# Kernel tuning notes

Hardware: AMD Instinct MI355X
Metric: run time of the kernel (lower is better)

## Reference

```python
import jax, jax.numpy as jnp
import numpy as np

B = 2048      # env batch (graphs)
A = 8         # agents per graph (fully connected)
N = B * A     # total nodes
DIN = 192     # raw obs dim
HD = 256      # h_dim (base MLP)
MD = 256      # mem_dim (GRU)
GD = 128      # gnn_dim (per-head GATv2 out, concat=False -> head mean)
H = 4         # GAT heads
NA = 20       # n_actions
ED = 3        # edge_dim


def setup_inputs() -> dict:
    key = jax.random.key(0)
    ks = jax.random.split(key, 16)
    # fully-connected directed graph per group of A agents, no self loops
    s, d = np.meshgrid(np.arange(A), np.arange(A), indexing='ij')
    mask = s != d
    s = s[mask]; d = d[mask]                     # [A*(A-1)]
    off = (np.arange(B) * A)[:, None]
    src = (off + s[None, :]).reshape(-1)
    dst = (off + d[None, :]).reshape(-1)
    edge_index = jnp.asarray(np.stack([src, dst]), dtype=jnp.int32)  # [2, E]
    E = src.shape[0]
    p = lambda k, sh: jax.random.normal(ks[k], sh, jnp.float32) * 0.02
    return {
        'inputs': jax.random.normal(ks[0], (N, DIN), jnp.float32),
        'hidden_states': jax.random.normal(ks[1], (N, MD), jnp.float32) * 0.1,
        'edge_index': edge_index,
        'edge_attr': jax.random.uniform(ks[2], (E, ED), jnp.float32),
        # base MLP (2 layers: Linear+ReLU+LayerNorm)
        'W1': p(3, (DIN, HD)), 'b1': jnp.zeros(HD), 'g1': jnp.ones(HD), 'be1': jnp.zeros(HD),
        'W2': p(4, (HD, HD)),  'b2': jnp.zeros(HD), 'g2': jnp.ones(HD), 'be2': jnp.zeros(HD),
        # GRUCell
        'Wih': p(5, (3 * MD, HD)), 'Whh': p(6, (3 * MD, MD)),
        'bih': jnp.zeros(3 * MD), 'bhh': jnp.zeros(3 * MD),
        # GATv2Conv (edge_dim=3, heads=4, concat=False, residual)
        'Wl': p(7, (MD, H * GD)), 'bl': jnp.zeros(H * GD),
        'Wr': p(8, (MD, H * GD)), 'br': jnp.zeros(H * GD),
        'att': p(9, (H, GD)),
        'We': p(10, (ED, H * GD)),
        'Wres': p(11, (MD, GD)),
        'bg': jnp.zeros(GD),
        # head: LayerNorm + Linear
        'lng': jnp.ones(GD), 'lnb': jnp.zeros(GD),
        'Wout': p(12, (GD, NA)), 'bout': jnp.zeros(NA),
    }


def _ln(x, g, b):
    mu = jnp.mean(x, -1, keepdims=True)
    xc = x - mu
    v = jnp.mean(xc * xc, -1, keepdims=True)
    return xc * jax.lax.rsqrt(v + 1e-5) * g + b


def _fwd(inputs, hidden_states, edge_attr, edge_index,
         W1, b1, g1, be1, W2, b2, g2, be2,
         Wih, Whh, bih, bhh,
         Wl, bl, Wr, br, att, We, Wres, bg,
         lng, lnb, Wout, bout):
    src, dst = edge_index[0], edge_index[1]
    # ---- base MLP encode ----
    x = _ln(jax.nn.relu(inputs @ W1 + b1), g1, be1)
    x = _ln(jax.nn.relu(x @ W2 + b2), g2, be2)          # [N, HD]
    # ---- SimpleConv(aggr='mean', combine_root='self_loop') ----
    s = jax.ops.segment_sum(x[src], dst, num_segments=N) + x
    deg = jax.ops.segment_sum(jnp.ones(src.shape[0], x.dtype), dst, num_segments=N) + 1.0
    x = s / deg[:, None]                                 # [N, HD]
    # ---- GRUCell ----
    gi = x @ Wih.T + bih
    gh = hidden_states @ Whh.T + bhh
    ir, iz, inn = jnp.split(gi, 3, -1)
    hr, hz, hn = jnp.split(gh, 3, -1)
    r = jax.nn.sigmoid(ir + hr)
    z = jax.nn.sigmoid(iz + hz)
    n = jnp.tanh(inn + r * hn)
    h = (1.0 - z) * n + z * hidden_states                # [N, MD]
    # ---- GATv2Conv (add self loops, edge_attr fill='mean') ----
    loop = jnp.arange(N, dtype=src.dtype)
    sf = jnp.concatenate([src, loop])
    df = jnp.concatenate([dst, loop])
    ea = jnp.concatenate([edge_attr, jnp.broadcast_to(edge_attr.mean(0), (N, ED))], 0)
    xl = (h @ Wl + bl).reshape(N, H, GD)
    xr = (h @ Wr + br).reshape(N, H, GD)
    m = xl[sf] + xr[df] + (ea @ We).reshape(-1, H, GD)   # [Ef, H, GD]
    m = jnp.where(m > 0, m, 0.2 * m)                     # leaky_relu(0.2)
    logits = jnp.einsum('ehc,hc->eh', m, att)            # [Ef, H]
    mx = jax.ops.segment_max(logits, df, num_segments=N)
    ex = jnp.exp(logits - mx[df])
    den = jax.ops.segment_sum(ex, df, num_segments=N)
    alpha = ex / (den[df] + 1e-16)                       # segment softmax
    out = jax.ops.segment_sum(xl[sf] * alpha[..., None], df, num_segments=N)
    out = out.mean(1) + h @ Wres + bg                    # head mean + residual + bias
    zg = jax.nn.relu(out)                                # [N, GD]
    # ---- action head ----
    q = _ln(zg, lng, lnb) @ Wout + bout                  # [N, NA]
    return q, h


def reference(inputs, hidden_states, edge_index, edge_attr,
              W1, b1, g1, be1, W2, b2, g2, be2,
              Wih, Whh, bih, bhh,
              Wl, bl, Wr, br, att, We, Wres, bg,
              lng, lnb, Wout, bout):
    return _fwd(inputs, hidden_states, edge_attr, edge_index,
                W1, b1, g1, be1, W2, b2, g2, be2,
                Wih, Whh, bih, bhh,
                Wl, bl, Wr, br, att, We, Wres, bg,
                lng, lnb, Wout, bout)
```

## Files before the change

### kernel.cpp

```cpp
#include <hip/hip_runtime.h>
#include <hip/hip_bf16.h>

constexpr int NB  = 2048;
constexpr int AG  = 8;
constexpr int NN  = NB * AG;
constexpr int DIN = 192;
constexpr int HD  = 256;
constexpr int MD  = 256;
constexpr int GD  = 128;
constexpr int NA  = 20;
constexpr int NE  = NB * AG * (AG - 1);

typedef __attribute__((ext_vector_type(8))) short bfrag8;
typedef __attribute__((ext_vector_type(4))) short sfrag4;
typedef __attribute__((ext_vector_type(4))) float f32x4;

#define MFMA16(a, b, c) __builtin_amdgcn_mfma_f32_16x16x32_bf16((a), (b), (c), 0, 0, 0)

__device__ __forceinline__ float bf2f(__hip_bfloat16 x) { return __bfloat162float(x); }
__device__ __forceinline__ __hip_bfloat16 f2bf(float x) { return __float2bfloat16(x); }
__device__ __forceinline__ short f2bs(float x) {
    __hip_bfloat16 b = __float2bfloat16(x);
    return *reinterpret_cast<short*>(&b);
}
__device__ __forceinline__ bfrag8 ldf(const __hip_bfloat16* p) { return *(const bfrag8*)p; }
__device__ __forceinline__ bfrag8 ldf32(const float* p) {
    const f32x4 a = *(const f32x4*)p;
    const f32x4 b = *(const f32x4*)(p + 4);
    bfrag8 r;
    r[0] = f2bs(a[0]); r[1] = f2bs(a[1]); r[2] = f2bs(a[2]); r[3] = f2bs(a[3]);
    r[4] = f2bs(b[0]); r[5] = f2bs(b[1]); r[6] = f2bs(b[2]); r[7] = f2bs(b[3]);
    return r;
}
__device__ __forceinline__ float sigmf(float x) { return 1.f / (1.f + __expf(-x)); }
__device__ __forceinline__ float blo(unsigned u) { return __uint_as_float(u << 16); }
__device__ __forceinline__ float bhi(unsigned u) { return __uint_as_float(u & 0xffff0000u); }

__global__ __launch_bounds__(256) void k_prep(
    const float* __restrict__ W1, const float* __restrict__ W2,
    const float* __restrict__ Wih, const float* __restrict__ Whh,
    const float* __restrict__ Wl, const float* __restrict__ bl,
    const float* __restrict__ Wr, const float* __restrict__ br,
    const float* __restrict__ Wres, const float* __restrict__ Wout,
    const float* __restrict__ ea,
    __hip_bfloat16* __restrict__ W1T, __hip_bfloat16* __restrict__ W2T,
    __hip_bfloat16* __restrict__ WihB, __hip_bfloat16* __restrict__ WhhB,
    __hip_bfloat16* __restrict__ WcatT, float* __restrict__ WoutTf,
    float* __restrict__ bcat, float* __restrict__ ea_partials)
{
    __shared__ float sw[4][3];
    const int tid = threadIdx.x;
    if (blockIdx.x >= 3151) {
        const int b = blockIdx.x - 3151;
        float a0 = 0.f, a1 = 0.f, a2 = 0.f;
#pragma unroll
        for (int k = 0; k < 7; k++) {
            int e = b * 1792 + k * 256 + tid;
            a0 += ea[e * 3 + 0];
            a1 += ea[e * 3 + 1];
            a2 += ea[e * 3 + 2];
        }
#pragma unroll
        for (int off = 1; off < 64; off <<= 1) {
            a0 += __shfl_xor(a0, off); a1 += __shfl_xor(a1, off); a2 += __shfl_xor(a2, off);
        }
        if ((tid & 63) == 0) { sw[tid >> 6][0] = a0; sw[tid >> 6][1] = a1; sw[tid >> 6][2] = a2; }
        __syncthreads();
        if (tid == 0) {
            ea_partials[b * 3 + 0] = sw[0][0] + sw[1][0] + sw[2][0] + sw[3][0];
            ea_partials[b * 3 + 1] = sw[0][1] + sw[1][1] + sw[2][1] + sw[3][1];
            ea_partials[b * 3 + 2] = sw[0][2] + sw[1][2] + sw[2][2] + sw[3][2];
        }
        return;
    }
    int i = blockIdx.x * 256 + tid;
    if (i < 49152) { int o = i / 192, c = i % 192; W1T[i] = f2bf(W1[c * 256 + o]); return; }
    i -= 49152;
    if (i < 65536) { int o = i >> 8, c = i & 255; W2T[i] = f2bf(W2[c * 256 + o]); return; }
    i -= 65536;
    if (i < 196608) { WihB[i] = f2bf(Wih[i]); return; }
    i -= 196608;
    if (i < 196608) { WhhB[i] = f2bf(Whh[i]); return; }
    i -= 196608;
    if (i < 294912) {
        int o = i >> 8, c = i & 255;
        float v;
        if (o < 512)       v = Wl[c * 512 + o];
        else if (o < 1024) v = Wr[c * 512 + (o - 512)];
        else               v = Wres[c * 128 + (o - 1024)];
        WcatT[i] = f2bf(v); return;
    }
    i -= 294912;
    if (i < 2560) { int o = i >> 7, c = i & 127; WoutTf[i] = Wout[c * 20 + o]; return; }
    i -= 2560;
    if (i < 1152) {
        float v = 0.f;
        if (i < 512) v = bl[i]; else if (i < 1024) v = br[i - 512];
        bcat[i] = v;
    }
}

__global__ __launch_bounds__(256) void k_encode(
    const float* __restrict__ in,
    const __hip_bfloat16* __restrict__ W1T,
    const float* __restrict__ b1, const float* __restrict__ g1, const float* __restrict__ be1,
    const __hip_bfloat16* __restrict__ W2T,
    const float* __restrict__ b2, const float* __restrict__ g2, const float* __restrict__ be2,
    __hip_bfloat16* __restrict__ xm)
{
    __shared__ float sf[16][257];
    __shared__ alignas(16) __hip_bfloat16 sb[16][264];
    const int tid = threadIdx.x;
    const int lane = tid & 63, w = tid >> 6;
    const int r = lane & 15, q = lane >> 4;
    const int m0 = blockIdx.x * 16;

    {
        bfrag8 af[6];
        const float* ap = in + (size_t)(m0 + r) * DIN + q * 8;
#pragma unroll
        for (int kb = 0; kb < 6; kb++) af[kb] = ldf32(ap + kb * 32);
#pragma unroll
        for (int i = 0; i < 4; i++) {
            int t = w * 4 + i;
            const __hip_bfloat16* wp = W1T + (size_t)(t * 16 + r) * DIN + q * 8;
            bfrag8 bf[6];
#pragma unroll
            for (int kb = 0; kb < 6; kb++) bf[kb] = ldf(wp + kb * 32);
            f32x4 acc = (f32x4){0.f, 0.f, 0.f, 0.f};
#pragma unroll
            for (int kb = 0; kb < 6; kb++) acc = MFMA16(af[kb], bf[kb], acc);
            int col = t * 16 + r;
            float bias = b1[col];
#pragma unroll
            for (int reg = 0; reg < 4; reg++)
                sf[q * 4 + reg][col] = fmaxf(acc[reg] + bias, 0.f);
        }
    }
    __syncthreads();
    {
        int rowi = tid >> 4, c16 = tid & 15;
        float vals[16]; float s = 0.f, s2 = 0.f;
#pragma unroll
        for (int j = 0; j < 16; j++) { float v = sf[rowi][c16 + 16 * j]; vals[j] = v; s += v; s2 += v * v; }
#pragma unroll
        for (int off = 1; off < 16; off <<= 1) { s += __shfl_xor(s, off); s2 += __shfl_xor(s2, off); }
        float mean = s * (1.f / HD);
        float var = fmaxf(s2 * (1.f / HD) - mean * mean, 0.f);
        float rs = rsqrtf(var + 1e-5f);
#pragma unroll
        for (int j = 0; j < 16; j++) {
            int col = c16 + 16 * j;
            sb[rowi][col] = f2bf((vals[j] - mean) * rs * g1[col] + be1[col]);
        }
    }
    __syncthreads();

    {
        bfrag8 af[8];
        const __hip_bfloat16* ap = &sb[r][0];
#pragma unroll
        for (int kb = 0; kb < 8; kb++) af[kb] = ldf(ap + kb * 32 + q * 8);
        float outv[4][4];
#pragma unroll
        for (int i = 0; i < 4; i++) {
            int t = w * 4 + i;
            const __hip_bfloat16* wp = W2T + (size_t)(t * 16 + r) * HD + q * 8;
            bfrag8 bf[8];
#pragma unroll
            for (int kb = 0; kb < 8; kb++) bf[kb] = ldf(wp + kb * 32);
            f32x4 acc = (f32x4){0.f, 0.f, 0.f, 0.f};
#pragma unroll
            for (int kb = 0; kb < 8; kb++) acc = MFMA16(af[kb], bf[kb], acc);
#pragma unroll
            for (int reg = 0; reg < 4; reg++) outv[i][reg] = acc[reg];
        }
        __syncthreads();
#pragma unroll
        for (int i = 0; i < 4; i++) {
            int col = (w * 4 + i) * 16 + r;
            float bias = b2[col];
#pragma unroll
            for (int reg = 0; reg < 4; reg++)
                sf[q * 4 + reg][col] = fmaxf(outv[i][reg] + bias, 0.f);
        }
    }
    __syncthreads();
    {
        int rowi = tid >> 4, c16 = tid & 15;
        float vals[16]; float s = 0.f, s2 = 0.f;
#pragma unroll
        for (int j = 0; j < 16; j++) { float v = sf[rowi][c16 + 16 * j]; vals[j] = v; s += v; s2 += v * v; }
#pragma unroll
        for (int off = 1; off < 16; off <<= 1) { s += __shfl_xor(s, off); s2 += __shfl_xor(s2, off); }
        float mean = s * (1.f / HD);
        float var = fmaxf(s2 * (1.f / HD) - mean * mean, 0.f);
        float rs = rsqrtf(var + 1e-5f);
#pragma unroll
        for (int j = 0; j < 16; j++) {
            int col = c16 + 16 * j;
            sb[rowi][col] = f2bf((vals[j] - mean) * rs * g2[col] + be2[col]);
        }
    }
    __syncthreads();
    {
        int col = tid;
        float a0 = 0.f, a1 = 0.f;
#pragma unroll
        for (int i = 0; i < 8; i++) { a0 += bf2f(sb[i][col]); a1 += bf2f(sb[8 + i][col]); }
        xm[(size_t)(2 * blockIdx.x) * HD + col] = f2bf(a0 * 0.125f);
        xm[(size_t)(2 * blockIdx.x + 1) * HD + col] = f2bf(a1 * 0.125f);
    }
}

__global__ __launch_bounds__(256) void k_gi(
    const __hip_bfloat16* __restrict__ xm,
    const __hip_bfloat16* __restrict__ WihB,
    const float* __restrict__ bih,
    float* __restrict__ gi)
{
    const int tid = threadIdx.x;
    const int lane = tid & 63, w = tid >> 6;
    const int r = lane & 15, q = lane >> 4;
    const int m0 = (blockIdx.x >> 1) * 16;
    const int t0 = (blockIdx.x & 1) * 24;

    bfrag8 af[8];
    const __hip_bfloat16* ap = xm + (size_t)(m0 + r) * MD + q * 8;
#pragma unroll
    for (int kb = 0; kb < 8; kb++) af[kb] = ldf(ap + kb * 32);
#pragma unroll
    for (int i = 0; i < 6; i++) {
        int t = t0 + w * 6 + i;
        const __hip_bfloat16* wp = WihB + (size_t)(t * 16 + r) * MD + q * 8;
        bfrag8 bf[8];
#pragma unroll
        for (int kb = 0; kb < 8; kb++) bf[kb] = ldf(wp + kb * 32);
        f32x4 acc = (f32x4){0.f, 0.f, 0.f, 0.f};
#pragma unroll
        for (int kb = 0; kb < 8; kb++) acc = MFMA16(af[kb], bf[kb], acc);
        int col = t * 16 + r;
        float bias = bih[col];
#pragma unroll
        for (int reg = 0; reg < 4; reg++) {
            int R = m0 + q * 4 + reg;
            gi[(size_t)R * 768 + col] = acc[reg] + bias;
        }
    }
}

__global__ __launch_bounds__(256, 3) void k_gatgru(
    const float* __restrict__ hprev,
    const __hip_bfloat16* __restrict__ WhhB,
    const float* __restrict__ bhh,
    const float* __restrict__ gi,
    const __hip_bfloat16* __restrict__ WcatT,
    const float* __restrict__ bcat,
    const float* __restrict__ ea,
    const float* __restrict__ ea_partials,
    const float* __restrict__ att,
    const float* __restrict__ We,
    const float* __restrict__ bg,
    const float* __restrict__ lng, const float* __restrict__ lnb,
    const float* __restrict__ WoutTf,
    const float* __restrict__ bout,
    float* __restrict__ hout,
    float* __restrict__ qout)
{
    __shared__ alignas(16) __hip_bfloat16 sx[16][1160];
    __shared__ alignas(16) unsigned char u_shszg[16 * 272 * 2];
    __shared__ float slog[2][4][8][8];
    __shared__ float smean[4];
    auto sh  = (__hip_bfloat16(*)[272])u_shszg;
    auto szg = (float(*)[136])u_shszg;
    const int tid = threadIdx.x;
    const int lane = tid & 63, w = tid >> 6;
    const int r = lane & 15, q = lane >> 4;
    const int m0 = blockIdx.x * 16;

    if (tid < 3) {
        float s = 0.f;
        for (int i = 0; i < 64; i++) s += ea_partials[i * 3 + tid];
        smean[tid] = s * (1.f / NE);
    }

    float vea[2][3];
    {
        int l = (lane < 56) ? lane : 0;
#pragma unroll
        for (int g = 0; g < 2; g++) {
            const float* ep = ea + (size_t)((blockIdx.x * 2 + g) * 56 + l) * 3;
            vea[g][0] = ep[0]; vea[g][1] = ep[1]; vea[g][2] = ep[2];
        }
    }

    {
        f32x4 aR[4], aZ[4], aN[4];
#pragma unroll
        for (int i = 0; i < 4; i++) {
            aR[i] = (f32x4){0.f, 0.f, 0.f, 0.f};
            aZ[i] = (f32x4){0.f, 0.f, 0.f, 0.f};
            aN[i] = (f32x4){0.f, 0.f, 0.f, 0.f};
        }
        const float* ap = hprev + (size_t)(m0 + r) * MD + q * 8;
#pragma unroll
        for (int kb = 0; kb < 8; kb++) {
            bfrag8 af = ldf32(ap + kb * 32);
#pragma unroll
            for (int i = 0; i < 4; i++) {
                int ct = w * 4 + i;
                bfrag8 bR = ldf(WhhB + (size_t)(ct * 16 + r) * MD + kb * 32 + q * 8);
                bfrag8 bZ = ldf(WhhB + (size_t)(256 + ct * 16 + r) * MD + kb * 32 + q * 8);
                bfrag8 bN = ldf(WhhB + (size_t)(512 + ct * 16 + r) * MD + kb * 32 + q * 8);
                aR[i] = MFMA16(af, bR, aR[i]);
                aZ[i] = MFMA16(af, bZ, aZ[i]);
                aN[i] = MFMA16(af, bN, aN[i]);
            }
        }
#pragma unroll
        for (int i = 0; i < 4; i++) {
            int c = (w * 4 + i) * 16 + r;
            float bhr = bhh[c], bhz = bhh[256 + c], bhn = bhh[512 + c];
#pragma unroll
            for (int reg = 0; reg < 4; reg++) {
                int R = m0 + q * 4 + reg;
                const float* gir = gi + (size_t)(R >> 3) * 768;
                float rr = sigmf(gir[c] + aR[i][reg] + bhr);
                float zz = sigmf(gir[256 + c] + aZ[i][reg] + bhz);
                float nn = tanhf(gir[512 + c] + rr * (aN[i][reg] + bhn));
                float hp = hprev[(size_t)R * MD + c];
                float hv = (1.f - zz) * nn + zz * hp;
                hout[(size_t)R * MD + c] = hv;
                sh[q * 4 + reg][c] = f2bf(hv);
            }
        }
    }
    __syncthreads();

    {
        bfrag8 afr[8];
#pragma unroll
        for (int kb = 0; kb < 8; kb++) afr[kb] = ldf(&sh[r][kb * 32 + q * 8]);
#pragma unroll
        for (int pass = 0; pass < 2; pass++) {
            f32x4 acc[9];
#pragma unroll
            for (int i = 0; i < 9; i++) acc[i] = (f32x4){0.f, 0.f, 0.f, 0.f};
#pragma unroll
            for (int kb = 0; kb < 8; kb++) {
#pragma unroll
                for (int i = 0; i < 9; i++) {
                    int t = pass * 36 + w * 9 + i;
                    bfrag8 bfv = ldf(WcatT + (size_t)(t * 16 + r) * MD + kb * 32 + q * 8);
                    acc[i] = MFMA16(bfv, afr[kb], acc[i]);
                }
            }
#pragma unroll
            for (int i = 0; i < 9; i++) {
                int fbase = (pass * 36 + w * 9 + i) * 16 + q * 4;
                sfrag4 pk;
#pragma unroll
                for (int reg = 0; reg < 4; reg++)
                    pk[reg] = f2bs(acc[i][reg] + bcat[fbase + reg]);
                *(sfrag4*)&sx[r][fbase] = pk;
            }
        }
    }
    __syncthreads();
    const float em0 = smean[0], em1 = smean[1], em2 = smean[2];

    {
        const int li = lane & 31, half = lane >> 5;
#pragma unroll
        for (int t = 0; t < 2; t++) {
            const int combo = w * 2 + t;
            const int gg = combo >> 2, hh = combo & 3;
            const f32x4 va  = *(const f32x4*)&att[hh * 128 + li * 4];
            const f32x4 vw0 = *(const f32x4*)&We[0 * 512 + hh * 128 + li * 4];
            const f32x4 vw1 = *(const f32x4*)&We[1 * 512 + hh * 128 + li * 4];
            const f32x4 vw2 = *(const f32x4*)&We[2 * 512 + hh * 128 + li * 4];
            float at0 = va[0],  at1 = va[1],  at2 = va[2],  at3 = va[3];
            float w00 = vw0[0], w01 = vw0[1], w02 = vw0[2], w03 = vw0[3];
            float w10 = vw1[0], w11 = vw1[1], w12 = vw1[2], w13 = vw1[3];
            float w20 = vw2[0], w21 = vw2[1], w22 = vw2[2], w23 = vw2[3];
            float ve0 = vea[gg][0], ve1 = vea[gg][1], ve2 = vea[gg][2];
            float xv[4][4];
#pragma unroll
            for (int sh2 = 0; sh2 < 4; sh2++) {
                int sL = sh2 * 2 + half;
                uint2 uxl = *(const uint2*)&sx[gg * 8 + sL][hh * 128 + li * 4];
                xv[sh2][0] = blo(uxl.x); xv[sh2][1] = bhi(uxl.x);
                xv[sh2][2] = blo(uxl.y); xv[sh2][3] = bhi(uxl.y);
            }
            float mylog = 0.f;
#pragma unroll
            for (int d = 0; d < 8; d++) {
                uint2 uxr = *(const uint2*)&sx[gg * 8 + d][512 + hh * 128 + li * 4];
                float xr0 = blo(uxr.x), xr1 = bhi(uxr.x), xr2 = blo(uxr.y), xr3 = bhi(uxr.y);
#pragma unroll
                for (int sh2 = 0; sh2 < 4; sh2++) {
                    int sL = sh2 * 2 + half;
                    int el = sL * 7 + d - (d > sL ? 1 : 0);
                    float e0 = __shfl(ve0, el), e1 = __shfl(ve1, el), e2 = __shfl(ve2, el);
                    bool slf = (sL == d);
                    e0 = slf ? em0 : e0; e1 = slf ? em1 : e1; e2 = slf ? em2 : e2;
                    float p, m;
                    m = fmaf(e2, w20, fmaf(e1, w10, fmaf(e0, w00, xv[sh2][0]))) + xr0;
                    m = fmaxf(m, 0.2f * m); p = m * at0;
                    m = fmaf(e2, w21, fmaf(e1, w11, fmaf(e0, w01, xv[sh2][1]))) + xr1;
                    m = fmaxf(m, 0.2f * m); p = fmaf(m, at1, p);
                    m = fmaf(e2, w22, fmaf(e1, w12, fmaf(e0, w02, xv[sh2][2]))) + xr2;
                    m = fmaxf(m, 0.2f * m); p = fmaf(m, at2, p);
                    m = fmaf(e2, w23, fmaf(e1, w13, fmaf(e0, w03, xv[sh2][3]))) + xr3;
                    m = fmaxf(m, 0.2f * m); p = fmaf(m, at3, p);
                    p += __shfl_xor(p, 1);  p += __shfl_xor(p, 2);  p += __shfl_xor(p, 4);
                    p += __shfl_xor(p, 8);  p += __shfl_xor(p, 16);
                    float got = __shfl(p, ((lane & 1) << 5) | li);
                    bool want = ((lane >> 3) == d) && (((lane & 7) >> 1) == sh2);
                    mylog = want ? got : mylog;
                }
            }
            ((float*)&slog[gg][hh][0][0])[lane] = mylog;
        }
    }
    __syncthreads();

    if (tid < 64) {
        int sg = tid >> 5, sh2 = (tid >> 3) & 3, d = tid & 7;
        float* L = &slog[sg][sh2][d][0];
        float mx = L[0];
#pragma unroll
        for (int s = 1; s < 8; s++) mx = fmaxf(mx, L[s]);
        float ex[8]; float den = 0.f;
#pragma unroll
        for (int s = 0; s < 8; s++) { ex[s] = __expf(L[s] - mx); den += ex[s]; }
        float inv = 1.f / (den + 1e-16f);
#pragma unroll
        for (int s = 0; s < 8; s++) L[s] = ex[s] * inv;
    }
    __syncthreads();

    {
        f32x4 acc0 = (f32x4){0.f, 0.f, 0.f, 0.f};
        f32x4 acc1 = (f32x4){0.f, 0.f, 0.f, 0.f};
        const int ggr = r >> 3, dr = r & 7;
#pragma unroll
        for (int ah = 0; ah < 4; ah++) {
            bfrag8 afA;
#pragma unroll
            for (int j = 0; j < 8; j++) {
                int k = q * 8 + j;
                float v = 0.f;
                if (k < 16) {
                    int ggk = k >> 3, s = k & 7;
                    if (ggk == ggr) v = slog[ggk][ah][dr][s];
                }
                afA[j] = f2bs(v);
            }
#pragma unroll
            for (int j2 = 0; j2 < 2; j2++) {
                int chunk = w * 2 + j2;
                bfrag8 bfB;
#pragma unroll
                for (int j = 0; j < 8; j++) {
                    int k = (q * 8 + j) & 15;
                    bfB[j] = *(const short*)&sx[k][ah * 128 + chunk * 16 + r];
                }
                if (j2 == 0) acc0 = MFMA16(afA, bfB, acc0);
                else         acc1 = MFMA16(afA, bfB, acc1);
            }
        }
#pragma unroll
        for (int j2 = 0; j2 < 2; j2++) {
            f32x4 a = j2 ? acc1 : acc0;
            int c = (w * 2 + j2) * 16 + r;
            float bgc = bg[c];
#pragma unroll
            for (int reg = 0; reg < 4; reg++) {
                int row = q * 4 + reg;
                float o = a[reg] * 0.25f + bf2f(sx[row][1024 + c]) + bgc;
                szg[row][c] = fmaxf(o, 0.f);
            }
        }
    }
    __syncthreads();

    {
        int row = tid >> 4, j = tid & 15;
        float v[8]; float s = 0.f, s2 = 0.f;
#pragma unroll
        for (int cj = 0; cj < 8; cj++) { v[cj] = szg[row][j + 16 * cj]; s += v[cj]; s2 += v[cj] * v[cj]; }
#pragma unroll
        for (int off = 1; off < 16; off <<= 1) { s += __shfl_xor(s, off); s2 += __shfl_xor(s2, off); }
        float mean = s * (1.f / GD);
        float var = fmaxf(s2 * (1.f / GD) - mean * mean, 0.f);
        float rs = rsqrtf(var + 1e-5f);
#pragma unroll
        for (int cj = 0; cj < 8; cj++) {
            int c = j + 16 * cj;
            szg[row][c] = (v[cj] - mean) * rs * lng[c] + lnb[c];
        }
    }
    __syncthreads();

    {
        int row = tid >> 4, j = tid & 15;
        for (int jj = j; jj < NA; jj += 16) {
            float a = bout[jj];
            const float* wo = WoutTf + jj * 128;
#pragma unroll
            for (int c4 = 0; c4 < 32; c4++) {
                f32x4 z = *(const f32x4*)&szg[row][c4 * 4];
                const f32x4 wv = *(const f32x4*)&wo[c4 * 4];
                a = fmaf(z[0], wv[0], a); a = fmaf(z[1], wv[1], a);
                a = fmaf(z[2], wv[2], a); a = fmaf(z[3], wv[3], a);
            }
            qout[(size_t)(m0 + row) * NA + jj] = a;
        }
    }
}

extern "C" void kernel_launch(void* const* d_in, const int* in_sizes, int n_in,
                              void* d_out, int out_size, void* d_ws, size_t ws_size,
                              hipStream_t stream) {
    const float* inp   = (const float*)d_in[0];
    const float* hid   = (const float*)d_in[1];
    const float* eatt  = (const float*)d_in[3];
    const float* W1    = (const float*)d_in[4];
    const float* b1    = (const float*)d_in[5];
    const float* g1    = (const float*)d_in[6];
    const float* be1   = (const float*)d_in[7];
    const float* W2    = (const float*)d_in[8];
    const float* b2    = (const float*)d_in[9];
    const float* g2    = (const float*)d_in[10];
    const float* be2   = (const float*)d_in[11];
    const float* Wih   = (const float*)d_in[12];
    const float* Whh   = (const float*)d_in[13];
    const float* bih   = (const float*)d_in[14];
    const float* bhh   = (const float*)d_in[15];
    const float* Wl    = (const float*)d_in[16];
    const float* bl    = (const float*)d_in[17];
    const float* Wr    = (const float*)d_in[18];
    const float* br    = (const float*)d_in[19];
    const float* att   = (const float*)d_in[20];
    const float* We    = (const float*)d_in[21];
    const float* Wres  = (const float*)d_in[22];
    const float* bg    = (const float*)d_in[23];
    const float* lng   = (const float*)d_in[24];
    const float* lnb   = (const float*)d_in[25];
    const float* Wout  = (const float*)d_in[26];
    const float* bout  = (const float*)d_in[27];

    float* qout = (float*)d_out;
    float* hout = (float*)d_out + (size_t)NN * NA;

    char* ws = (char*)d_ws;
    float*           ea_partials = (float*)ws;
    __hip_bfloat16*  xm    = (__hip_bfloat16*)(ws + 2048);
    float*           gi    = (float*)(ws + 1050624);
    __hip_bfloat16*  W1T   = (__hip_bfloat16*)(ws + 7342080);
    __hip_bfloat16*  W2T   = (__hip_bfloat16*)(ws + 7440384);
    __hip_bfloat16*  WihB  = (__hip_bfloat16*)(ws + 7571456);
    __hip_bfloat16*  WhhB  = (__hip_bfloat16*)(ws + 7964672);
    __hip_bfloat16*  WcatT = (__hip_bfloat16*)(ws + 8357888);
    float*           bcat  = (float*)(ws + 8947712);
    float*           WoutTf= (float*)(ws + 8952320);

    k_prep<<<3215, 256, 0, stream>>>(W1, W2, Wih, Whh, Wl, bl, Wr, br, Wres, Wout, eatt,
                                     W1T, W2T, WihB, WhhB, WcatT, WoutTf, bcat, ea_partials);
    k_encode<<<NN / 16, 256, 0, stream>>>(inp, W1T, b1, g1, be1, W2T, b2, g2, be2, xm);
    k_gi<<<256, 256, 0, stream>>>(xm, WihB, bih, gi);
    k_gatgru<<<NN / 16, 256, 0, stream>>>(hid, WhhB, bhh, gi, WcatT, bcat, eatt,
                                          ea_partials, att, We, bg, lng, lnb,
                                          WoutTf, bout, hout, qout);
}
```

Baseline: 354.7 us.

## Software-pipeline weight loads in GRU and GAT GEMMs and stage gi in LDS

Double-buffers the global weight-fragment loads in both the GRU hidden GEMM and the GATv2 projection GEMM, prefetching the next k-block while MFMAs run on the current one. Preloads all hprev A fragments up front and caches the per-graph gi rows in shared memory instead of reading them repeatedly from global. To fit the extra live registers, the occupancy hint drops from 3 to 2 blocks per CU, which costs latency hiding across waves.

New measurement: 331.3 us. 6.6% less time.

```diff
diff --git a/kernel.cpp b/kernel.cpp
--- a/kernel.cpp
+++ b/kernel.cpp
@@ -249,7 +249,7 @@
     }
 }
 
-__global__ __launch_bounds__(256, 3) void k_gatgru(
+__global__ __launch_bounds__(256, 2) void k_gatgru(
     const float* __restrict__ hprev,
     const __hip_bfloat16* __restrict__ WhhB,
     const float* __restrict__ bhh,
@@ -270,6 +270,7 @@
     __shared__ alignas(16) __hip_bfloat16 sx[16][1160];
     __shared__ alignas(16) unsigned char u_shszg[16 * 272 * 2];
     __shared__ float slog[2][4][8][8];
+    __shared__ float sgi[2][768];
     __shared__ float smean[4];
     auto sh  = (__hip_bfloat16(*)[272])u_shszg;
     auto szg = (float(*)[136])u_shszg;
@@ -283,6 +284,11 @@
         for (int i = 0; i < 64; i++) s += ea_partials[i * 3 + tid];
         smean[tid] = s * (1.f / NE);
     }
+    {
+        const float* gsrc = gi + (size_t)(blockIdx.x * 2) * 768;
+#pragma unroll
+        for (int k = 0; k < 6; k++) ((float*)sgi)[k * 256 + tid] = gsrc[k * 256 + tid];
+    }
 
     float vea[2][3];
     {
@@ -293,28 +299,38 @@
             vea[g][0] = ep[0]; vea[g][1] = ep[1]; vea[g][2] = ep[2];
         }
     }
-
-    {
-        f32x4 aR[4], aZ[4], aN[4];
-#pragma unroll
-        for (int i = 0; i < 4; i++) {
-            aR[i] = (f32x4){0.f, 0.f, 0.f, 0.f};
-            aZ[i] = (f32x4){0.f, 0.f, 0.f, 0.f};
-            aN[i] = (f32x4){0.f, 0.f, 0.f, 0.f};
-        }
+    __syncthreads();
+
+    {
+        bfrag8 afr[8];
         const float* ap = hprev + (size_t)(m0 + r) * MD + q * 8;
 #pragma unroll
+        for (int kb = 0; kb < 8; kb++) afr[kb] = ldf32(ap + kb * 32);
+        f32x4 acc[12];
+#pragma unroll
+        for (int i = 0; i < 12; i++) acc[i] = (f32x4){0.f, 0.f, 0.f, 0.f};
+        const __hip_bfloat16* wb = WhhB + (size_t)r * MD + q * 8;
+        bfrag8 bcur[12], bnxt[12];
+#pragma unroll
+        for (int i = 0; i < 4; i++)
+#pragma unroll
+            for (int g3 = 0; g3 < 3; g3++)
+                bcur[i * 3 + g3] = ldf(wb + (size_t)((g3 * 256 + (w * 4 + i) * 16)) * MD);
+#pragma unroll
         for (int kb = 0; kb < 8; kb++) {
-            bfrag8 af = ldf32(ap + kb * 32);
-#pragma unroll
-            for (int i = 0; i < 4; i++) {
-                int ct = w * 4 + i;
-                bfrag8 bR = ldf(WhhB + (size_t)(ct * 16 + r) * MD + kb * 32 + q * 8);
-                bfrag8 bZ = ldf(WhhB + (size_t)(256 + ct * 16 + r) * MD + kb * 32 + q * 8);
-                bfrag8 bN = ldf(WhhB + (size_t)(512 + ct * 16 + r) * MD + kb * 32 + q * 8);
-                aR[i] = MFMA16(af, bR, aR[i]);
-                aZ[i] = MFMA16(af, bZ, aZ[i]);
-                aN[i] = MFMA16(af, bN, aN[i]);
+            if (kb < 7) {
+#pragma unroll
+                for (int i = 0; i < 4; i++)
+#pragma unroll
+                    for (int g3 = 0; g3 < 3; g3++)
+                        bnxt[i * 3 + g3] = ldf(wb + (size_t)((g3 * 256 + (w * 4 + i) * 16)) * MD
+                                               + (kb + 1) * 32);
+            }
+#pragma unroll
+            for (int j = 0; j < 12; j++) acc[j] = MFMA16(afr[kb], bcur[j], acc[j]);
+            if (kb < 7) {
+#pragma unroll
+                for (int j = 0; j < 12; j++) bcur[j] = bnxt[j];
             }
         }
 #pragma unroll
@@ -324,10 +340,10 @@
 #pragma unroll
             for (int reg = 0; reg < 4; reg++) {
                 int R = m0 + q * 4 + reg;
-                const float* gir = gi + (size_t)(R >> 3) * 768;
-                float rr = sigmf(gir[c] + aR[i][reg] + bhr);
-                float zz = sigmf(gir[256 + c] + aZ[i][reg] + bhz);
-                float nn = tanhf(gir[512 + c] + rr * (aN[i][reg] + bhn));
+                const float* gir = &sgi[(q * 4 + reg) >> 3][0];
+                float rr = sigmf(gir[c] + acc[i * 3 + 0][reg] + bhr);
+                float zz = sigmf(gir[256 + c] + acc[i * 3 + 1][reg] + bhz);
+                float nn = tanhf(gir[512 + c] + rr * (acc[i * 3 + 2][reg] + bhn));
                 float hp = hprev[(size_t)R * MD + c];
                 float hv = (1.f - zz) * nn + zz * hp;
                 hout[(size_t)R * MD + c] = hv;
@@ -343,21 +359,32 @@
         for (int kb = 0; kb < 8; kb++) afr[kb] = ldf(&sh[r][kb * 32 + q * 8]);
 #pragma unroll
         for (int pass = 0; pass < 2; pass++) {
+            const int tb = pass * 36 + w * 9;
             f32x4 acc[9];
 #pragma unroll
             for (int i = 0; i < 9; i++) acc[i] = (f32x4){0.f, 0.f, 0.f, 0.f};
+            const __hip_bfloat16* wb = WcatT + (size_t)r * MD + q * 8;
+            bfrag8 bcur[9], bnxt[9];
+#pragma unroll
+            for (int i = 0; i < 9; i++)
+                bcur[i] = ldf(wb + (size_t)((tb + i) * 16) * MD);
 #pragma unroll
             for (int kb = 0; kb < 8; kb++) {
-#pragma unroll
-                for (int i = 0; i < 9; i++) {
-                    int t = pass * 36 + w * 9 + i;
-                    bfrag8 bfv = ldf(WcatT + (size_t)(t * 16 + r) * MD + kb * 32 + q * 8);
-                    acc[i] = MFMA16(bfv, afr[kb], acc[i]);
+                if (kb < 7) {
+#pragma unroll
+                    for (int i = 0; i < 9; i++)
+                        bnxt[i] = ldf(wb + (size_t)((tb + i) * 16) * MD + (kb + 1) * 32);
                 }
+#pragma unroll
+                for (int i = 0; i < 9; i++) acc[i] = MFMA16(bcur[i], afr[kb], acc[i]);
+                if (kb < 7) {
+#pragma unroll
+                    for (int i = 0; i < 9; i++) bcur[i] = bnxt[i];
+                }
             }
 #pragma unroll
             for (int i = 0; i < 9; i++) {
-                int fbase = (pass * 36 + w * 9 + i) * 16 + q * 4;
+                int fbase = (tb + i) * 16 + q * 4;
                 sfrag4 pk;
 #pragma unroll
                 for (int reg = 0; reg < 4; reg++)
```

## Split fused GRU+GAT kernel into tiled GRU GEMM, projection GEMM, and GAT kernels

Applied to the files above, without the earlier changes.

Breaks the monolithic per-16-node kernel into three launches. The GRU hidden matmul and the concatenated Wl/Wr/Wres projection each become 128-row-tiled GEMM kernels, so every weight fragment loaded feeds many more MFMAs. The GAT kernel then reads the bf16 projection from a global workspace into shared memory. The aim is to cut redundant weight traffic from the 16-row tiles. The cost is extra global round-trips for h and the 1152-wide projection, plus two more launches.

Result: faster. 329.9 us (-7.0%).

```diff
diff --git a/kernel.cpp b/kernel.cpp
--- a/kernel.cpp
+++ b/kernel.cpp
@@ -249,13 +249,130 @@
     }
 }
 
-__global__ __launch_bounds__(256, 3) void k_gatgru(
+__global__ __launch_bounds__(256, 2) void k_gruG(
     const float* __restrict__ hprev,
     const __hip_bfloat16* __restrict__ WhhB,
     const float* __restrict__ bhh,
     const float* __restrict__ gi,
+    float* __restrict__ hout)
+{
+    const int tid = threadIdx.x;
+    const int lane = tid & 63, w = tid >> 6;
+    const int r = lane & 15, q = lane >> 4;
+    const int m0 = (blockIdx.x >> 2) * 128;
+    const int cg = (blockIdx.x & 3) * 64;
+
+    bfrag8 afr[2][8];
+#pragma unroll
+    for (int t = 0; t < 2; t++) {
+        const float* ap = hprev + (size_t)(m0 + (w * 2 + t) * 16 + r) * MD + q * 8;
+#pragma unroll
+        for (int kb = 0; kb < 8; kb++) afr[t][kb] = ldf32(ap + kb * 32);
+    }
+    f32x4 acc[2][12];
+#pragma unroll
+    for (int t = 0; t < 2; t++)
+#pragma unroll
+        for (int n = 0; n < 12; n++) acc[t][n] = (f32x4){0.f, 0.f, 0.f, 0.f};
+
+#pragma unroll
+    for (int kb = 0; kb < 8; kb++) {
+        bfrag8 bfB[12];
+#pragma unroll
+        for (int g = 0; g < 3; g++)
+#pragma unroll
+            for (int nj = 0; nj < 4; nj++)
+                bfB[g * 4 + nj] = ldf(WhhB + (size_t)(g * 256 + cg + nj * 16 + r) * MD
+                                      + kb * 32 + q * 8);
+#pragma unroll
+        for (int t = 0; t < 2; t++)
+#pragma unroll
+            for (int n = 0; n < 12; n++)
+                acc[t][n] = MFMA16(bfB[n], afr[t][kb], acc[t][n]);
+    }
+
+#pragma unroll
+    for (int t = 0; t < 2; t++) {
+        int node = m0 + (w * 2 + t) * 16 + r;
+        const float* gir = gi + (size_t)(node >> 3) * 768;
+#pragma unroll
+        for (int nj = 0; nj < 4; nj++) {
+            int c = cg + nj * 16 + q * 4;
+            f32x4 gR = *(const f32x4*)&gir[c];
+            f32x4 gZ = *(const f32x4*)&gir[256 + c];
+            f32x4 gN = *(const f32x4*)&gir[512 + c];
+            f32x4 bR = *(const f32x4*)&bhh[c];
+            f32x4 bZ = *(const f32x4*)&bhh[256 + c];
+            f32x4 bN = *(const f32x4*)&bhh[512 + c];
+            f32x4 hp = *(const f32x4*)&hprev[(size_t)node * MD + c];
+            f32x4 hv;
+#pragma unroll
+            for (int reg = 0; reg < 4; reg++) {
+                float rr = sigmf(gR[reg] + acc[t][0 + nj][reg] + bR[reg]);
+                float zz = sigmf(gZ[reg] + acc[t][4 + nj][reg] + bZ[reg]);
+                float nn = tanhf(gN[reg] + rr * (acc[t][8 + nj][reg] + bN[reg]));
+                hv[reg] = (1.f - zz) * nn + zz * hp[reg];
+            }
+            *(f32x4*)&hout[(size_t)node * MD + c] = hv;
+        }
+    }
+}
+
+__global__ __launch_bounds__(256, 2) void k_xlr(
+    const float* __restrict__ h,
     const __hip_bfloat16* __restrict__ WcatT,
     const float* __restrict__ bcat,
+    __hip_bfloat16* __restrict__ xlr)
+{
+    const int tid = threadIdx.x;
+    const int lane = tid & 63, w = tid >> 6;
+    const int r = lane & 15, q = lane >> 4;
+    const int m0 = (blockIdx.x / 9) * 128;
+    const int nb = (blockIdx.x % 9) * 128;
+
+    bfrag8 afr[2][8];
+#pragma unroll
+    for (int t = 0; t < 2; t++) {
+        const float* ap = h + (size_t)(m0 + (w * 2 + t) * 16 + r) * MD + q * 8;
+#pragma unroll
+        for (int kb = 0; kb < 8; kb++) afr[t][kb] = ldf32(ap + kb * 32);
+    }
+    f32x4 acc[2][8];
+#pragma unroll
+    for (int t = 0; t < 2; t++)
+#pragma unroll
+        for (int n = 0; n < 8; n++) acc[t][n] = (f32x4){0.f, 0.f, 0.f, 0.f};
+
+#pragma unroll
+    for (int kb = 0; kb < 8; kb++) {
+        bfrag8 bfB[8];
+#pragma unroll
+        for (int nj = 0; nj < 8; nj++)
+            bfB[nj] = ldf(WcatT + (size_t)(nb + nj * 16 + r) * MD + kb * 32 + q * 8);
+#pragma unroll
+        for (int t = 0; t < 2; t++)
+#pragma unroll
+            for (int n = 0; n < 8; n++)
+                acc[t][n] = MFMA16(bfB[n], afr[t][kb], acc[t][n]);
+    }
+
+#pragma unroll
+    for (int t = 0; t < 2; t++) {
+        int node = m0 + (w * 2 + t) * 16 + r;
+#pragma unroll
+        for (int nj = 0; nj < 8; nj++) {
+            int fb = nb + nj * 16 + q * 4;
+            sfrag4 pk;
+#pragma unroll
+            for (int reg = 0; reg < 4; reg++)
+                pk[reg] = f2bs(acc[t][nj][reg] + bcat[fb + reg]);
+            *(sfrag4*)&xlr[(size_t)node * 1152 + fb] = pk;
+        }
+    }
+}
+
+__global__ __launch_bounds__(256) void k_gat(
+    const __hip_bfloat16* __restrict__ xlr,
     const float* __restrict__ ea,
     const float* __restrict__ ea_partials,
     const float* __restrict__ att,
@@ -264,15 +381,12 @@
     const float* __restrict__ lng, const float* __restrict__ lnb,
     const float* __restrict__ WoutTf,
     const float* __restrict__ bout,
-    float* __restrict__ hout,
     float* __restrict__ qout)
 {
     __shared__ alignas(16) __hip_bfloat16 sx[16][1160];
-    __shared__ alignas(16) unsigned char u_shszg[16 * 272 * 2];
+    __shared__ alignas(16) float szg[16][136];
     __shared__ float slog[2][4][8][8];
     __shared__ float smean[4];
-    auto sh  = (__hip_bfloat16(*)[272])u_shszg;
-    auto szg = (float(*)[136])u_shszg;
     const int tid = threadIdx.x;
     const int lane = tid & 63, w = tid >> 6;
     const int r = lane & 15, q = lane >> 4;
@@ -283,6 +397,10 @@
         for (int i = 0; i < 64; i++) s += ea_partials[i * 3 + tid];
         smean[tid] = s * (1.f / NE);
     }
+    for (int idx = tid; idx < 2304; idx += 256) {
+        int row = idx / 144, off = (idx % 144) * 8;
+        *(uint4*)&sx[row][off] = *(const uint4*)&xlr[(size_t)(m0 + row) * 1152 + off];
+    }
 
     float vea[2][3];
     {
@@ -291,79 +409,6 @@
         for (int g = 0; g < 2; g++) {
             const float* ep = ea + (size_t)((blockIdx.x * 2 + g) * 56 + l) * 3;
             vea[g][0] = ep[0]; vea[g][1] = ep[1]; vea[g][2] = ep[2];
-        }
-    }
-
-    {
-        f32x4 aR[4], aZ[4], aN[4];
-#pragma unroll
-        for (int i = 0; i < 4; i++) {
-            aR[i] = (f32x4){0.f, 0.f, 0.f, 0.f};
-            aZ[i] = (f32x4){0.f, 0.f, 0.f, 0.f};
-            aN[i] = (f32x4){0.f, 0.f, 0.f, 0.f};
-        }
-        const float* ap = hprev + (size_t)(m0 + r) * MD + q * 8;
-#pragma unroll
-        for (int kb = 0; kb < 8; kb++) {
-            bfrag8 af = ldf32(ap + kb * 32);
-#pragma unroll
-            for (int i = 0; i < 4; i++) {
-                int ct = w * 4 + i;
-                bfrag8 bR = ldf(WhhB + (size_t)(ct * 16 + r) * MD + kb * 32 + q * 8);
-                bfrag8 bZ = ldf(WhhB + (size_t)(256 + ct * 16 + r) * MD + kb * 32 + q * 8);
-                bfrag8 bN = ldf(WhhB + (size_t)(512 + ct * 16 + r) * MD + kb * 32 + q * 8);
-                aR[i] = MFMA16(af, bR, aR[i]);
-                aZ[i] = MFMA16(af, bZ, aZ[i]);
-                aN[i] = MFMA16(af, bN, aN[i]);
-            }
-        }
-#pragma unroll
-        for (int i = 0; i < 4; i++) {
-            int c = (w * 4 + i) * 16 + r;
-            float bhr = bhh[c], bhz = bhh[256 + c], bhn = bhh[512 + c];
-#pragma unroll
-            for (int reg = 0; reg < 4; reg++) {
-                int R = m0 + q * 4 + reg;
-                const float* gir = gi + (size_t)(R >> 3) * 768;
-                float rr = sigmf(gir[c] + aR[i][reg] + bhr);
-                float zz = sigmf(gir[256 + c] + aZ[i][reg] + bhz);
-                float nn = tanhf(gir[512 + c] + rr * (aN[i][reg] + bhn));
-                float hp = hprev[(size_t)R * MD + c];
-                float hv = (1.f - zz) * nn + zz * hp;
-                hout[(size_t)R * MD + c] = hv;
-                sh[q * 4 + reg][c] = f2bf(hv);
-            }
-        }
-    }
-    __syncthreads();
-
-    {
-        bfrag8 afr[8];
-#pragma unroll
-        for (int kb = 0; kb < 8; kb++) afr[kb] = ldf(&sh[r][kb * 32 + q * 8]);
-#pragma unroll
-        for (int pass = 0; pass < 2; pass++) {
-            f32x4 acc[9];
-#pragma unroll
-            for (int i = 0; i < 9; i++) acc[i] = (f32x4){0.f, 0.f, 0.f, 0.f};
-#pragma unroll
-            for (int kb = 0; kb < 8; kb++) {
-#pragma unroll
-                for (int i = 0; i < 9; i++) {
-                    int t = pass * 36 + w * 9 + i;
-                    bfrag8 bfv = ldf(WcatT + (size_t)(t * 16 + r) * MD + kb * 32 + q * 8);
-                    acc[i] = MFMA16(bfv, afr[kb], acc[i]);
-                }
-            }
-#pragma unroll
-            for (int i = 0; i < 9; i++) {
-                int fbase = (pass * 36 + w * 9 + i) * 16 + q * 4;
-                sfrag4 pk;
-#pragma unroll
-                for (int reg = 0; reg < 4; reg++)
-                    pk[reg] = f2bs(acc[i][reg] + bcat[fbase + reg]);
-                *(sfrag4*)&sx[r][fbase] = pk;
-            }
         }
     }
     __syncthreads();
@@ -565,12 +610,14 @@
     __hip_bfloat16*  WcatT = (__hip_bfloat16*)(ws + 8357888);
     float*           bcat  = (float*)(ws + 8947712);
     float*           WoutTf= (float*)(ws + 8952320);
+    __hip_bfloat16*  xlr   = (__hip_bfloat16*)(ws + 8962560);
 
     k_prep<<<3215, 256, 0, stream>>>(W1, W2, Wih, Whh, Wl, bl, Wr, br, Wres, Wout, eatt,
                                      W1T, W2T, WihB, WhhB, WcatT, WoutTf, bcat, ea_partials);
     k_encode<<<NN / 16, 256, 0, stream>>>(inp, W1T, b1, g1, be1, W2T, b2, g2, be2, xm);
     k_gi<<<256, 256, 0, stream>>>(xm, WihB, bih, gi);
-    k_gatgru<<<NN / 16, 256, 0, stream>>>(hid, WhhB, bhh, gi, WcatT, bcat, eatt,
-                                          ea_partials, att, We, bg, lng, lnb,
-                                          WoutTf, bout, hout, qout);
-}
+    k_gruG<<<512, 256, 0, stream>>>(hid, WhhB, bhh, gi, hout);
+    k_xlr<<<1152, 256, 0, stream>>>(hout, WcatT, bcat, xlr);
+    k_gat<<<NN / 16, 256, 0, stream>>>(xlr, eatt, ea_partials, att, We, bg,
+                                       lng, lnb, WoutTf, bout, qout);
+}
```
